# Optimization experiments

Measured on AMD Instinct MI355X. Metric: run time of the kernel, lower is better.

Reference implementation:

```python
import jax, jax.numpy as jnp
import numpy as np

B, Q, KV = 4, 256, 1024
QS, KS, H, VS = 128, 128, 128, 256

def setup_inputs() -> dict:
    key = jax.random.key(0)
    ks = jax.random.split(key, 7)
    return {
        "queries": jax.random.normal(ks[0], (B, Q, QS), dtype=jnp.float32),
        "keys": jax.random.normal(ks[1], (B, KV, KS), dtype=jnp.float32),
        "values": jax.random.normal(ks[2], (B, KV, VS), dtype=jnp.float32),
        "valid_lens": jax.random.randint(ks[3], (B,), 0, KV, dtype=jnp.int64 if jax.config.read('jax_enable_x64') else jnp.int32),
        "Wq": jax.random.normal(ks[4], (QS, H), dtype=jnp.float32),
        "Wk": jax.random.normal(ks[5], (KS, H), dtype=jnp.float32),
        "wv": jax.random.normal(ks[6], (H,), dtype=jnp.float32),
    }

def reference(queries, keys, values, valid_lens, Wq, Wk, wv):
    # project: [B,Q,H], [B,KV,H]
    q = jnp.einsum('bqd,dh->bqh', queries, Wq)
    k = jnp.einsum('bkd,dh->bkh', keys, Wk)
    # additive scores: broadcast add -> tanh -> reduce with w_v  [B,Q,KV]
    feats = jnp.tanh(q[:, :, None, :] + k[:, None, :, :])  # [B,Q,KV,H]
    scores = jnp.einsum('bqkh,h->bqk', feats, wv)
    # masked softmax over KV with value -1e6 at masked slots
    mask = jnp.arange(scores.shape[-1])[None, None, :] < valid_lens[:, None, None]
    scores = jnp.where(mask, scores, -1e6)
    attn = jax.nn.softmax(scores, axis=-1)
    # weighted sum of values  [B,Q,VS]
    return jnp.einsum('bqk,bkv->bqv', attn, values)
```

## Files before the change

kernel.cpp:

```cpp
#include <hip/hip_runtime.h>

#define C2LOG2E 2.8853900817779268f
#define LOG2E   1.4426950408889634f

__device__ __forceinline__ float sig2(float x) {
    return __builtin_amdgcn_rcpf(__builtin_amdgcn_exp2f(x) + 1.0f);
}

__global__ __launch_bounds__(256) void proj_kernel(
    const float* __restrict__ q_in, const float* __restrict__ k_in,
    const float* __restrict__ Wq, const float* __restrict__ Wk,
    const int* __restrict__ valid_lens,
    float* __restrict__ qc, float* __restrict__ kct)
{
    __shared__ __align__(16) float x_s[8][128];
    __shared__ __align__(16) float ps[4][8][128];
    int tid = threadIdx.x;
    int blk = blockIdx.x;
    bool is_q = (blk < 128);
    int r0 = (is_q ? blk : blk - 128) * 8;
    int bb = r0 >> 10;
    if (!is_q) {
        int vl = valid_lens[bb];
        if ((r0 & 1023) >= vl) return;
    }
    const float* X = (is_q ? q_in : k_in) + (size_t)r0 * 128;
    const float* W = is_q ? Wq : Wk;

    *(float4*)&x_s[tid >> 5][(tid & 31) * 4] = ((const float4*)X)[tid];
    __syncthreads();

    int hl = tid & 63;
    int dq = tid >> 6;
    float a0[8] = {0,0,0,0,0,0,0,0};
    float a1[8] = {0,0,0,0,0,0,0,0};
#pragma unroll
    for (int i4 = 0; i4 < 8; ++i4) {
        int d = dq*32 + i4*4;
        float w00 = W[(d+0)*128 + hl], w01 = W[(d+0)*128 + hl + 64];
        float w10 = W[(d+1)*128 + hl], w11 = W[(d+1)*128 + hl + 64];
        float w20 = W[(d+2)*128 + hl], w21 = W[(d+2)*128 + hl + 64];
        float w30 = W[(d+3)*128 + hl], w31 = W[(d+3)*128 + hl + 64];
#pragma unroll
        for (int r = 0; r < 8; ++r) {
            float4 xv = *(const float4*)&x_s[r][d];
            a0[r] = fmaf(xv.x,w00, fmaf(xv.y,w10, fmaf(xv.z,w20, fmaf(xv.w,w30, a0[r]))));
            a1[r] = fmaf(xv.x,w01, fmaf(xv.y,w11, fmaf(xv.z,w21, fmaf(xv.w,w31, a1[r]))));
        }
    }
#pragma unroll
    for (int r = 0; r < 8; ++r) {
        ps[dq][r][hl]      = a0[r];
        ps[dq][r][hl + 64] = a1[r];
    }
    __syncthreads();

    int r  = tid >> 5;
    int c4 = (tid & 31) * 4;
    float4 s0 = *(const float4*)&ps[0][r][c4];
    float4 s1 = *(const float4*)&ps[1][r][c4];
    float4 s2 = *(const float4*)&ps[2][r][c4];
    float4 s3 = *(const float4*)&ps[3][r][c4];
    float4 v = make_float4(((s0.x+s1.x)+(s2.x+s3.x))*C2LOG2E,
                           ((s0.y+s1.y)+(s2.y+s3.y))*C2LOG2E,
                           ((s0.z+s1.z)+(s2.z+s3.z))*C2LOG2E,
                           ((s0.w+s1.w)+(s2.w+s3.w))*C2LOG2E);
    if (is_q) {
        *(float4*)&qc[(size_t)(r0 + r)*128 + c4] = v;
    } else {
        int c    = (r0 & 1023) >> 6;
        int kvin = (r0 & 63) + r;
        *(float4*)&kct[((((size_t)(bb*16 + c))*32 + (c4 >> 2))*64 + kvin)*4] = v;
    }
}

__global__ __launch_bounds__(512, 8) void attn_split_kernel(
    const float* __restrict__ qc, const float* __restrict__ kct,
    const float* __restrict__ values, const int* __restrict__ valid_lens,
    const float* __restrict__ wv, float* __restrict__ pO, float* __restrict__ pml)
{
    __shared__ float2 e2_s[512];
    __shared__ float4 po[8][2][64];
    __shared__ float2 red_m[8], red_s[8];

    int tid  = threadIdx.x;
    int b    = blockIdx.y;
    int q0   = blockIdx.x * 2;
    int s    = blockIdx.z;
    int w    = tid >> 6;
    int lane = tid & 63;
    int vl   = valid_lens[b];
    int row0 = b*256 + q0;

    if (s == 1 && vl > 0 && vl <= 512) {
        if (tid < 2) pml[(size_t)(1024 + row0 + tid)*2] = -1e30f;
        return;
    }

    const float4* qa4 = (const float4*)(qc + (size_t)row0*128);
    const float4* qb4 = qa4 + 32;
    const float4* wv4 = (const float4*)wv;
    const float4* p0  = (const float4*)kct + ((size_t)(b*16 + s*8 + w))*2048 + lane;

    float a00 = 0.f, a10 = 0.f;
    if ((s*8 + w)*64 < vl) {
#pragma unroll 4
        for (int hb = 0; hb < 32; ++hb) {
            float4 wvv = wv4[hb];
            float4 qa = qa4[hb], qb = qb4[hb];
            float4 k0 = p0[(size_t)hb*64];
            a00 = fmaf(wvv.x, sig2(qa.x + k0.x), a00);
            a10 = fmaf(wvv.x, sig2(qb.x + k0.x), a10);
            a00 = fmaf(wvv.y, sig2(qa.y + k0.y), a00);
            a10 = fmaf(wvv.y, sig2(qb.y + k0.y), a10);
            a00 = fmaf(wvv.z, sig2(qa.z + k0.z), a00);
            a10 = fmaf(wvv.z, sig2(qb.z + k0.z), a10);
            a00 = fmaf(wvv.w, sig2(qa.w + k0.w), a00);
            a10 = fmaf(wvv.w, sig2(qb.w + k0.w), a10);
        }
    }

    int lkv = w*64 + lane;
    bool valid = (s*512 + lkv < vl);
    float s00 = valid ? -2.f*a00 : -1e6f;
    float s10 = valid ? -2.f*a10 : -1e6f;

    float m0 = s00, m1 = s10;
#pragma unroll
    for (int off = 32; off; off >>= 1) {
        m0 = fmaxf(m0, __shfl_xor(m0, off));
        m1 = fmaxf(m1, __shfl_xor(m1, off));
    }
    if (lane == 0) red_m[w] = make_float2(m0, m1);
    __syncthreads();
    {
        float2 mm = red_m[0];
#pragma unroll
        for (int ww = 1; ww < 8; ++ww) {
            float2 t = red_m[ww];
            mm.x = fmaxf(mm.x, t.x); mm.y = fmaxf(mm.y, t.y);
        }
        m0 = mm.x; m1 = mm.y;
    }

    float e00 = __builtin_amdgcn_exp2f((s00 - m0) * LOG2E);
    float e10 = __builtin_amdgcn_exp2f((s10 - m1) * LOG2E);
    e2_s[lkv] = make_float2(e00, e10);
    float l0 = e00, l1 = e10;
#pragma unroll
    for (int off = 32; off; off >>= 1) {
        l0 += __shfl_xor(l0, off);
        l1 += __shfl_xor(l1, off);
    }
    if (lane == 0) red_s[w] = make_float2(l0, l1);
    __syncthreads();

    int local_end = (vl == 0) ? 512 : min(512, vl - s*512);
    float4 ac0 = {0,0,0,0}, ac1 = {0,0,0,0};
    const float4* V4 = (const float4*)values + (size_t)b*65536 + (size_t)s*512*64 + lane;
#pragma unroll 2
    for (int k2 = w; k2 < local_end; k2 += 8) {
        float4 vv = V4[(size_t)k2*64];
        float2 ee = e2_s[k2];
        ac0.x = fmaf(ee.x, vv.x, ac0.x); ac0.y = fmaf(ee.x, vv.y, ac0.y);
        ac0.z = fmaf(ee.x, vv.z, ac0.z); ac0.w = fmaf(ee.x, vv.w, ac0.w);
        ac1.x = fmaf(ee.y, vv.x, ac1.x); ac1.y = fmaf(ee.y, vv.y, ac1.y);
        ac1.z = fmaf(ee.y, vv.z, ac1.z); ac1.w = fmaf(ee.y, vv.w, ac1.w);
    }
    po[w][0][lane] = ac0;
    po[w][1][lane] = ac1;

    if (tid < 2) {
        float lsum = 0.f;
#pragma unroll
        for (int ww = 0; ww < 8; ++ww) {
            float2 t = red_s[ww];
            lsum += tid ? t.y : t.x;
        }
        float mm = tid ? m1 : m0;
        *(float2*)&pml[(size_t)(s*1024 + row0 + tid)*2] = make_float2(mm, lsum);
    }
    __syncthreads();

    int qq  = tid >> 8;
    int col = tid & 255;
    const float* pp = (const float*)po;
    float r = 0.f;
#pragma unroll
    for (int ww = 0; ww < 8; ++ww) r += pp[(ww*2 + qq)*256 + col];
    pO[(size_t)(s*1024 + row0 + qq)*256 + col] = r;
}

__global__ __launch_bounds__(256) void combine_kernel(
    const float* __restrict__ pO, const float* __restrict__ pml,
    float* __restrict__ out)
{
    int tid  = threadIdx.x;
    int row  = blockIdx.x*4 + (tid >> 6);
    int lane = tid & 63;
    float2 ml0 = *(const float2*)&pml[(size_t)row*2];
    float2 ml1 = *(const float2*)&pml[(size_t)(1024 + row)*2];
    float m  = fmaxf(ml0.x, ml1.x);
    float w0 = __builtin_amdgcn_exp2f((ml0.x - m) * LOG2E);
    float w1 = __builtin_amdgcn_exp2f((ml1.x - m) * LOG2E);
    float inv = 1.0f / (w0*ml0.y + w1*ml1.y);
    float4 o0 = ((const float4*)pO)[(size_t)row*64 + lane];
    float4 o1 = ((const float4*)pO)[(size_t)(1024 + row)*64 + lane];
    float4 o;
    o.x = (w0*o0.x + w1*o1.x) * inv;
    o.y = (w0*o0.y + w1*o1.y) * inv;
    o.z = (w0*o0.z + w1*o1.z) * inv;
    o.w = (w0*o0.w + w1*o1.w) * inv;
    ((float4*)out)[(size_t)row*64 + lane] = o;
}

extern "C" void kernel_launch(void* const* d_in, const int* in_sizes, int n_in,
                              void* d_out, int out_size, void* d_ws, size_t ws_size,
                              hipStream_t stream)
{
    const float* queries = (const float*)d_in[0];
    const float* keys    = (const float*)d_in[1];
    const float* values  = (const float*)d_in[2];
    const int*   vlens   = (const int*)d_in[3];
    const float* Wq      = (const float*)d_in[4];
    const float* Wk      = (const float*)d_in[5];
    const float* wv      = (const float*)d_in[6];
    float* out = (float*)d_out;

    float* qc  = (float*)d_ws;
    float* kct = qc  + 4*256*128;
    float* pO  = kct + 4*16*32*64*4;
    float* pml = pO  + 2*1024*256;

    proj_kernel<<<640, 256, 0, stream>>>(queries, keys, Wq, Wk, vlens, qc, kct);
    attn_split_kernel<<<dim3(128, 4, 2), 512, 0, stream>>>(qc, kct, values, vlens, wv, pO, pml);
    combine_kernel<<<256, 256, 0, stream>>>(pO, pml, out);
}
```

Baseline: 95.08 us.

## Split KV four ways and give each attention block four queries

The attention kernel now splits KV into four chunks of 256 instead of two of 512, and each block handles four queries. The block's eight warps form two groups of four, one per query pair, each scoring its 256-key chunk. In the P·V phase every loaded value row is reused across four queries instead of two, halving V reads per query, and the finer split lets blocks past valid_len exit early. The combine kernel now merges four partial softmax states instead of two, so partial-output traffic and workspace use grow.

```diff
diff --git a/kernel.cpp b/kernel.cpp
--- a/kernel.cpp
+++ b/kernel.cpp
@@ -79,31 +79,34 @@
     const float* __restrict__ values, const int* __restrict__ valid_lens,
     const float* __restrict__ wv, float* __restrict__ pO, float* __restrict__ pml)
 {
-    __shared__ float2 e2_s[512];
-    __shared__ float4 po[8][2][64];
+    __shared__ float2 e2_s[2][256];
+    __shared__ float4 po[8][4][64];
     __shared__ float2 red_m[8], red_s[8];
 
     int tid  = threadIdx.x;
     int b    = blockIdx.y;
-    int q0   = blockIdx.x * 2;
+    int q0   = blockIdx.x * 4;
     int s    = blockIdx.z;
     int w    = tid >> 6;
     int lane = tid & 63;
+    int qh   = w >> 2;
+    int c    = w & 3;
     int vl   = valid_lens[b];
     int row0 = b*256 + q0;
 
-    if (s == 1 && vl > 0 && vl <= 512) {
-        if (tid < 2) pml[(size_t)(1024 + row0 + tid)*2] = -1e30f;
+    if (vl > 0 && s*256 >= vl) {
+        if (tid < 4) pml[(size_t)(s*1024 + row0 + tid)*2] = -1e30f;
         return;
     }
 
-    const float4* qa4 = (const float4*)(qc + (size_t)row0*128);
+    const float4* qa4 = (const float4*)(qc + (size_t)(row0 + 2*qh)*128);
     const float4* qb4 = qa4 + 32;
     const float4* wv4 = (const float4*)wv;
-    const float4* p0  = (const float4*)kct + ((size_t)(b*16 + s*8 + w))*2048 + lane;
+    int chunk = s*4 + c;
+    const float4* p0 = (const float4*)kct + ((size_t)(b*16 + chunk))*2048 + lane;
 
     float a00 = 0.f, a10 = 0.f;
-    if ((s*8 + w)*64 < vl) {
+    if (chunk*64 < vl) {
 #pragma unroll 4
         for (int hb = 0; hb < 32; ++hb) {
             float4 wvv = wv4[hb];
@@ -120,8 +123,8 @@
         }
     }
 
-    int lkv = w*64 + lane;
-    bool valid = (s*512 + lkv < vl);
+    int lkv = c*64 + lane;
+    bool valid = (s*256 + lkv < vl);
     float s00 = valid ? -2.f*a00 : -1e6f;
     float s10 = valid ? -2.f*a10 : -1e6f;
 
@@ -134,10 +137,10 @@
     if (lane == 0) red_m[w] = make_float2(m0, m1);
     __syncthreads();
     {
-        float2 mm = red_m[0];
-#pragma unroll
-        for (int ww = 1; ww < 8; ++ww) {
-            float2 t = red_m[ww];
+        float2 mm = red_m[qh*4];
+#pragma unroll
+        for (int ww = 1; ww < 4; ++ww) {
+            float2 t = red_m[qh*4 + ww];
             mm.x = fmaxf(mm.x, t.x); mm.y = fmaxf(mm.y, t.y);
         }
         m0 = mm.x; m1 = mm.y;
@@ -145,7 +148,7 @@
 
     float e00 = __builtin_amdgcn_exp2f((s00 - m0) * LOG2E);
     float e10 = __builtin_amdgcn_exp2f((s10 - m1) * LOG2E);
-    e2_s[lkv] = make_float2(e00, e10);
+    e2_s[qh][lkv] = make_float2(e00, e10);
     float l0 = e00, l1 = e10;
 #pragma unroll
     for (int off = 32; off; off >>= 1) {
@@ -155,40 +158,50 @@
     if (lane == 0) red_s[w] = make_float2(l0, l1);
     __syncthreads();
 
-    int local_end = (vl == 0) ? 512 : min(512, vl - s*512);
-    float4 ac0 = {0,0,0,0}, ac1 = {0,0,0,0};
-    const float4* V4 = (const float4*)values + (size_t)b*65536 + (size_t)s*512*64 + lane;
+    int local_end = (vl == 0) ? 256 : min(256, vl - s*256);
+    float4 ac[4] = {{0,0,0,0},{0,0,0,0},{0,0,0,0},{0,0,0,0}};
+    const float4* V4 = (const float4*)values + (size_t)b*65536 + (size_t)s*256*64 + lane;
 #pragma unroll 2
     for (int k2 = w; k2 < local_end; k2 += 8) {
         float4 vv = V4[(size_t)k2*64];
-        float2 ee = e2_s[k2];
-        ac0.x = fmaf(ee.x, vv.x, ac0.x); ac0.y = fmaf(ee.x, vv.y, ac0.y);
-        ac0.z = fmaf(ee.x, vv.z, ac0.z); ac0.w = fmaf(ee.x, vv.w, ac0.w);
-        ac1.x = fmaf(ee.y, vv.x, ac1.x); ac1.y = fmaf(ee.y, vv.y, ac1.y);
-        ac1.z = fmaf(ee.y, vv.z, ac1.z); ac1.w = fmaf(ee.y, vv.w, ac1.w);
-    }
-    po[w][0][lane] = ac0;
-    po[w][1][lane] = ac1;
-
-    if (tid < 2) {
-        float lsum = 0.f;
-#pragma unroll
-        for (int ww = 0; ww < 8; ++ww) {
-            float2 t = red_s[ww];
-            lsum += tid ? t.y : t.x;
-        }
-        float mm = tid ? m1 : m0;
+        float2 ea = e2_s[0][k2];
+        float2 eb = e2_s[1][k2];
+        ac[0].x = fmaf(ea.x, vv.x, ac[0].x); ac[0].y = fmaf(ea.x, vv.y, ac[0].y);
+        ac[0].z = fmaf(ea.x, vv.z, ac[0].z); ac[0].w = fmaf(ea.x, vv.w, ac[0].w);
+        ac[1].x = fmaf(ea.y, vv.x, ac[1].x); ac[1].y = fmaf(ea.y, vv.y, ac[1].y);
+        ac[1].z = fmaf(ea.y, vv.z, ac[1].z); ac[1].w = fmaf(ea.y, vv.w, ac[1].w);
+        ac[2].x = fmaf(eb.x, vv.x, ac[2].x); ac[2].y = fmaf(eb.x, vv.y, ac[2].y);
+        ac[2].z = fmaf(eb.x, vv.z, ac[2].z); ac[2].w = fmaf(eb.x, vv.w, ac[2].w);
+        ac[3].x = fmaf(eb.y, vv.x, ac[3].x); ac[3].y = fmaf(eb.y, vv.y, ac[3].y);
+        ac[3].z = fmaf(eb.y, vv.z, ac[3].z); ac[3].w = fmaf(eb.y, vv.w, ac[3].w);
+    }
+#pragma unroll
+    for (int q = 0; q < 4; ++q) po[w][q][lane] = ac[q];
+
+    if (tid < 4) {
+        int rqh = tid >> 1;
+        float mm = -1e30f, lsum = 0.f;
+#pragma unroll
+        for (int ww = 0; ww < 4; ++ww) {
+            float2 tm = red_m[rqh*4 + ww];
+            float2 tl = red_s[rqh*4 + ww];
+            mm   = fmaxf(mm, (tid & 1) ? tm.y : tm.x);
+            lsum += (tid & 1) ? tl.y : tl.x;
+        }
         *(float2*)&pml[(size_t)(s*1024 + row0 + tid)*2] = make_float2(mm, lsum);
     }
     __syncthreads();
 
-    int qq  = tid >> 8;
-    int col = tid & 255;
+    int qq  = tid >> 7;
+    int col = (tid & 127) * 2;
     const float* pp = (const float*)po;
-    float r = 0.f;
-#pragma unroll
-    for (int ww = 0; ww < 8; ++ww) r += pp[(ww*2 + qq)*256 + col];
-    pO[(size_t)(s*1024 + row0 + qq)*256 + col] = r;
+    float rx = 0.f, ry = 0.f;
+#pragma unroll
+    for (int ww = 0; ww < 8; ++ww) {
+        float2 p = *(const float2*)&pp[(ww*4 + qq)*256 + col];
+        rx += p.x; ry += p.y;
+    }
+    *(float2*)&pO[(size_t)(s*1024 + row0 + qq)*256 + col] = make_float2(rx, ry);
 }
 
 __global__ __launch_bounds__(256) void combine_kernel(
@@ -198,19 +211,28 @@
     int tid  = threadIdx.x;
     int row  = blockIdx.x*4 + (tid >> 6);
     int lane = tid & 63;
-    float2 ml0 = *(const float2*)&pml[(size_t)row*2];
-    float2 ml1 = *(const float2*)&pml[(size_t)(1024 + row)*2];
-    float m  = fmaxf(ml0.x, ml1.x);
-    float w0 = __builtin_amdgcn_exp2f((ml0.x - m) * LOG2E);
-    float w1 = __builtin_amdgcn_exp2f((ml1.x - m) * LOG2E);
-    float inv = 1.0f / (w0*ml0.y + w1*ml1.y);
-    float4 o0 = ((const float4*)pO)[(size_t)row*64 + lane];
-    float4 o1 = ((const float4*)pO)[(size_t)(1024 + row)*64 + lane];
-    float4 o;
-    o.x = (w0*o0.x + w1*o1.x) * inv;
-    o.y = (w0*o0.y + w1*o1.y) * inv;
-    o.z = (w0*o0.z + w1*o1.z) * inv;
-    o.w = (w0*o0.w + w1*o1.w) * inv;
+    float2 ml[4];
+    float m = -1e30f;
+#pragma unroll
+    for (int s = 0; s < 4; ++s) {
+        ml[s] = *(const float2*)&pml[(size_t)(s*1024 + row)*2];
+        m = fmaxf(m, ml[s].x);
+    }
+    float ws[4], denom = 0.f;
+#pragma unroll
+    for (int s = 0; s < 4; ++s) {
+        ws[s] = __builtin_amdgcn_exp2f((ml[s].x - m) * LOG2E);
+        denom = fmaf(ws[s], ml[s].y, denom);
+    }
+    float inv = 1.0f / denom;
+    float4 o = {0,0,0,0};
+#pragma unroll
+    for (int s = 0; s < 4; ++s) {
+        float4 os = ((const float4*)pO)[(size_t)(s*1024 + row)*64 + lane];
+        o.x = fmaf(ws[s], os.x, o.x); o.y = fmaf(ws[s], os.y, o.y);
+        o.z = fmaf(ws[s], os.z, o.z); o.w = fmaf(ws[s], os.w, o.w);
+    }
+    o.x *= inv; o.y *= inv; o.z *= inv; o.w *= inv;
     ((float4*)out)[(size_t)row*64 + lane] = o;
 }
 
@@ -230,9 +252,9 @@
     float* qc  = (float*)d_ws;
     float* kct = qc  + 4*256*128;
     float* pO  = kct + 4*16*32*64*4;
-    float* pml = pO  + 2*1024*256;
+    float* pml = pO  + 4*1024*256;
 
     proj_kernel<<<640, 256, 0, stream>>>(queries, keys, Wq, Wk, vlens, qc, kct);
-    attn_split_kernel<<<dim3(128, 4, 2), 512, 0, stream>>>(qc, kct, values, vlens, wv, pO, pml);
+    attn_split_kernel<<<dim3(64, 4, 4), 512, 0, stream>>>(qc, kct, values, vlens, wv, pO, pml);
     combine_kernel<<<256, 256, 0, stream>>>(pO, pml, out);
 }
```

Result: slower. 99.95 us (+5.1%).

## Split KV into four chunks and share each score across two waves over H

Applied to the files above, without the earlier changes.

The KV axis is now split into four 256-wide chunks instead of two 512-wide ones. Each pair of waves splits the H reduction for one 64-key chunk and combines the halves through shared memory. Blocks whose chunk lies wholly past valid_len exit early, so the grid gives finer load balance across batches with uneven valid lengths. The cost is an extra barrier, twice as many partial outputs in workspace, and a four-way combine step.

```diff
diff --git a/kernel.cpp b/kernel.cpp
--- a/kernel.cpp
+++ b/kernel.cpp
@@ -79,33 +79,39 @@
     const float* __restrict__ values, const int* __restrict__ valid_lens,
     const float* __restrict__ wv, float* __restrict__ pO, float* __restrict__ pml)
 {
-    __shared__ float2 e2_s[512];
+    __shared__ float2 e2_s[256];
+    __shared__ float2 part[8][64];
     __shared__ float4 po[8][2][64];
-    __shared__ float2 red_m[8], red_s[8];
+    __shared__ float2 red_m[4], red_s[4];
 
     int tid  = threadIdx.x;
+    int w    = __builtin_amdgcn_readfirstlane(tid) >> 6;
+    int lane = tid & 63;
     int b    = blockIdx.y;
     int q0   = blockIdx.x * 2;
     int s    = blockIdx.z;
-    int w    = tid >> 6;
-    int lane = tid & 63;
     int vl   = valid_lens[b];
     int row0 = b*256 + q0;
 
-    if (s == 1 && vl > 0 && vl <= 512) {
-        if (tid < 2) pml[(size_t)(1024 + row0 + tid)*2] = -1e30f;
+    if (vl > 0 && s*256 >= vl) {
+        if (tid < 2) pml[(size_t)(s*1024 + row0 + tid)*2] = -1e30f;
         return;
     }
 
-    const float4* qa4 = (const float4*)(qc + (size_t)row0*128);
+    int c  = w >> 1;
+    int hh = w & 1;
+    int cg = s*4 + c;
+
+    const float4* qa4 = (const float4*)(qc + (size_t)row0*128) + hh*16;
     const float4* qb4 = qa4 + 32;
-    const float4* wv4 = (const float4*)wv;
-    const float4* p0  = (const float4*)kct + ((size_t)(b*16 + s*8 + w))*2048 + lane;
+    const float4* wv4 = (const float4*)wv + hh*16;
+    const float4* p0  = (const float4*)kct
+                      + (((size_t)(b*16 + cg))*32 + hh*16)*64 + lane;
 
     float a00 = 0.f, a10 = 0.f;
-    if ((s*8 + w)*64 < vl) {
+    if (cg*64 < vl) {
 #pragma unroll 4
-        for (int hb = 0; hb < 32; ++hb) {
+        for (int hb = 0; hb < 16; ++hb) {
             float4 wvv = wv4[hb];
             float4 qa = qa4[hb], qb = qb4[hb];
             float4 k0 = p0[(size_t)hb*64];
@@ -119,9 +125,15 @@
             a10 = fmaf(wvv.w, sig2(qb.w + k0.w), a10);
         }
     }
-
-    int lkv = w*64 + lane;
-    bool valid = (s*512 + lkv < vl);
+    part[w][lane] = make_float2(a00, a10);
+    __syncthreads();
+    {
+        float2 o = part[w ^ 1][lane];
+        a00 += o.x; a10 += o.y;
+    }
+
+    int lkv = c*64 + lane;
+    bool valid = (s*256 + lkv < vl);
     float s00 = valid ? -2.f*a00 : -1e6f;
     float s10 = valid ? -2.f*a10 : -1e6f;
 
@@ -131,13 +143,13 @@
         m0 = fmaxf(m0, __shfl_xor(m0, off));
         m1 = fmaxf(m1, __shfl_xor(m1, off));
     }
-    if (lane == 0) red_m[w] = make_float2(m0, m1);
+    if (hh == 0 && lane == 0) red_m[c] = make_float2(m0, m1);
     __syncthreads();
     {
         float2 mm = red_m[0];
 #pragma unroll
-        for (int ww = 1; ww < 8; ++ww) {
-            float2 t = red_m[ww];
+        for (int cc = 1; cc < 4; ++cc) {
+            float2 t = red_m[cc];
             mm.x = fmaxf(mm.x, t.x); mm.y = fmaxf(mm.y, t.y);
         }
         m0 = mm.x; m1 = mm.y;
@@ -145,19 +157,30 @@
 
     float e00 = __builtin_amdgcn_exp2f((s00 - m0) * LOG2E);
     float e10 = __builtin_amdgcn_exp2f((s10 - m1) * LOG2E);
-    e2_s[lkv] = make_float2(e00, e10);
+    if (hh == 0) e2_s[lkv] = make_float2(e00, e10);
     float l0 = e00, l1 = e10;
 #pragma unroll
     for (int off = 32; off; off >>= 1) {
         l0 += __shfl_xor(l0, off);
         l1 += __shfl_xor(l1, off);
     }
-    if (lane == 0) red_s[w] = make_float2(l0, l1);
-    __syncthreads();
-
-    int local_end = (vl == 0) ? 512 : min(512, vl - s*512);
+    if (hh == 0 && lane == 0) red_s[c] = make_float2(l0, l1);
+    __syncthreads();
+
+    if (tid < 2) {
+        float lsum = 0.f;
+#pragma unroll
+        for (int cc = 0; cc < 4; ++cc) {
+            float2 t = red_s[cc];
+            lsum += tid ? t.y : t.x;
+        }
+        float mm = tid ? m1 : m0;
+        *(float2*)&pml[(size_t)(s*1024 + row0 + tid)*2] = make_float2(mm, lsum);
+    }
+
+    int local_end = (vl == 0) ? 256 : min(256, vl - s*256);
     float4 ac0 = {0,0,0,0}, ac1 = {0,0,0,0};
-    const float4* V4 = (const float4*)values + (size_t)b*65536 + (size_t)s*512*64 + lane;
+    const float4* V4 = (const float4*)values + (size_t)b*65536 + (size_t)s*256*64 + lane;
 #pragma unroll 2
     for (int k2 = w; k2 < local_end; k2 += 8) {
         float4 vv = V4[(size_t)k2*64];
@@ -169,17 +192,6 @@
     }
     po[w][0][lane] = ac0;
     po[w][1][lane] = ac1;
-
-    if (tid < 2) {
-        float lsum = 0.f;
-#pragma unroll
-        for (int ww = 0; ww < 8; ++ww) {
-            float2 t = red_s[ww];
-            lsum += tid ? t.y : t.x;
-        }
-        float mm = tid ? m1 : m0;
-        *(float2*)&pml[(size_t)(s*1024 + row0 + tid)*2] = make_float2(mm, lsum);
-    }
     __syncthreads();
 
     int qq  = tid >> 8;
@@ -198,19 +210,28 @@
     int tid  = threadIdx.x;
     int row  = blockIdx.x*4 + (tid >> 6);
     int lane = tid & 63;
-    float2 ml0 = *(const float2*)&pml[(size_t)row*2];
-    float2 ml1 = *(const float2*)&pml[(size_t)(1024 + row)*2];
-    float m  = fmaxf(ml0.x, ml1.x);
-    float w0 = __builtin_amdgcn_exp2f((ml0.x - m) * LOG2E);
-    float w1 = __builtin_amdgcn_exp2f((ml1.x - m) * LOG2E);
-    float inv = 1.0f / (w0*ml0.y + w1*ml1.y);
-    float4 o0 = ((const float4*)pO)[(size_t)row*64 + lane];
-    float4 o1 = ((const float4*)pO)[(size_t)(1024 + row)*64 + lane];
-    float4 o;
-    o.x = (w0*o0.x + w1*o1.x) * inv;
-    o.y = (w0*o0.y + w1*o1.y) * inv;
-    o.z = (w0*o0.z + w1*o1.z) * inv;
-    o.w = (w0*o0.w + w1*o1.w) * inv;
+    float2 ml[4];
+    float m = -1e30f;
+#pragma unroll
+    for (int s = 0; s < 4; ++s) {
+        ml[s] = *(const float2*)&pml[(size_t)(s*1024 + row)*2];
+        m = fmaxf(m, ml[s].x);
+    }
+    float ws[4], denom = 0.f;
+#pragma unroll
+    for (int s = 0; s < 4; ++s) {
+        ws[s] = __builtin_amdgcn_exp2f((ml[s].x - m) * LOG2E);
+        denom = fmaf(ws[s], ml[s].y, denom);
+    }
+    float inv = 1.0f / denom;
+    float4 o = {0,0,0,0};
+#pragma unroll
+    for (int s = 0; s < 4; ++s) {
+        float4 os = ((const float4*)pO)[(size_t)(s*1024 + row)*64 + lane];
+        o.x = fmaf(ws[s], os.x, o.x); o.y = fmaf(ws[s], os.y, o.y);
+        o.z = fmaf(ws[s], os.z, o.z); o.w = fmaf(ws[s], os.w, o.w);
+    }
+    o.x *= inv; o.y *= inv; o.z *= inv; o.w *= inv;
     ((float4*)out)[(size_t)row*64 + lane] = o;
 }
 
@@ -230,9 +251,9 @@
     float* qc  = (float*)d_ws;
     float* kct = qc  + 4*256*128;
     float* pO  = kct + 4*16*32*64*4;
-    float* pml = pO  + 2*1024*256;
+    float* pml = pO  + 4*1024*256;
 
     proj_kernel<<<640, 256, 0, stream>>>(queries, keys, Wq, Wk, vlens, qc, kct);
-    attn_split_kernel<<<dim3(128, 4, 2), 512, 0, stream>>>(qc, kct, values, vlens, wv, pO, pml);
+    attn_split_kernel<<<dim3(128, 4, 4), 512, 0, stream>>>(qc, kct, values, vlens, wv, pO, pml);
     combine_kernel<<<256, 256, 0, stream>>>(pO, pml, out);
 }
```

Result: no change. 96.11 us (+1.1%).
